# Kernel tuning notes

Measured on AMD Instinct MI355X. Metric: run time of the kernel, lower is better.

The kernel has to match this reference:

```python
import jax, jax.numpy as jnp
import numpy as np

EMBED_DIM = 1024
NUM_HEADS = 16
HEAD_DIM = EMBED_DIM // NUM_HEADS


def setup_inputs() -> dict:
    key = jax.random.key(0)
    ks = jax.random.split(key, 9)
    B, S, D = 2, 2048, EMBED_DIM
    s = 1.0 / np.sqrt(D)
    x = jax.random.normal(ks[0], (B, S, D), dtype=jnp.float32)
    Wq = jax.random.uniform(ks[1], (D, D), jnp.float32, -s, s)
    bq = jax.random.uniform(ks[2], (D,), jnp.float32, -s, s)
    Wk = jax.random.uniform(ks[3], (D, D), jnp.float32, -s, s)
    bk = jax.random.uniform(ks[4], (D,), jnp.float32, -s, s)
    Wv = jax.random.uniform(ks[5], (D, D), jnp.float32, -s, s)
    bv = jax.random.uniform(ks[6], (D,), jnp.float32, -s, s)
    Wo = jax.random.uniform(ks[7], (D, D), jnp.float32, -s, s)
    bo = jax.random.uniform(ks[8], (D,), jnp.float32, -s, s)
    return {"x": x, "Wq": Wq, "bq": bq, "Wk": Wk, "bk": bk,
            "Wv": Wv, "bv": bv, "Wo": Wo, "bo": bo}


def reference(x, Wq, bq, Wk, bk, Wv, bv, Wo, bo):
    B, S, D = x.shape
    H, Hd = NUM_HEADS, HEAD_DIM
    # projections (torch Linear: y = x W^T + b); split heads -> [B, H, S, Hd]
    def split(t):
        return t.reshape(B, S, H, Hd).transpose(0, 2, 1, 3)
    Q = split(x @ Wq.T + bq)
    K = split(x @ Wk.T + bk)
    V = split(x @ Wv.T + bv)
    scores = jnp.einsum('bhqd,bhkd->bhqk', Q, K) / jnp.sqrt(jnp.float32(Hd))
    weights = jax.nn.softmax(scores, axis=-1)
    out = jnp.einsum('bhqk,bhkd->bhqd', weights, V)
    out = out.transpose(0, 2, 1, 3).reshape(B, S, D)
    return out @ Wo.T + bo
```

## Files before the change

kernel.cpp:

```cpp
#include <hip/hip_runtime.h>

typedef float f32x4  __attribute__((ext_vector_type(4)));
typedef float f32x16 __attribute__((ext_vector_type(16)));
typedef short bh8    __attribute__((ext_vector_type(8)));
typedef unsigned int u32;

#define MFMA16(a, b, c) __builtin_amdgcn_mfma_f32_16x16x32_bf16(a, b, c, 0, 0, 0)
#define MFMA32(a, b, c) __builtin_amdgcn_mfma_f32_32x32x16_bf16(a, b, c, 0, 0, 0)

#define BB 2
#define SS 2048
#define DD 1024
#define HH 16
#define HDIM 64
#define TT (BB * SS)

#define QSCALE 0.18033688011f

__device__ __forceinline__ unsigned short f2bf(float f) {
  unsigned u = __float_as_uint(f);
  u += 0x7fffu + ((u >> 16) & 1u);
  return (unsigned short)(u >> 16);
}
__device__ __forceinline__ float bf2f(short h) {
  return __uint_as_float(((u32)(unsigned short)h) << 16);
}
__device__ __forceinline__ u32 cvtpk(float lo, float hi) {
  u32 r;
  asm("v_cvt_pk_bf16_f32 %0, %1, %2" : "=v"(r) : "v"(lo), "v"(hi));
  return r;
}
#define PLSWAP(a, b) \
  asm("v_permlane32_swap_b32 %0, %1" : "+v"(a), "+v"(b))

__device__ __forceinline__ void gload_lds16(const void* gsrc, const void* ldst) {
  __builtin_amdgcn_global_load_lds(
      (const __attribute__((address_space(1))) unsigned int*)(unsigned long long)gsrc,
      (__attribute__((address_space(3))) unsigned int*)(unsigned int)(unsigned long long)ldst,
      16, 0, 0);
}

__global__ void cvt_all(const float* __restrict__ x,
                        const float* __restrict__ w0, const float* __restrict__ w1,
                        const float* __restrict__ w2, const float* __restrict__ w3,
                        unsigned short* __restrict__ xb,
                        unsigned short* __restrict__ wb) {
  const int b = blockIdx.x;
  const float* src;
  unsigned short* dst;
  int i;
  if (b < 2048) {
    src = x; dst = xb;
    i = b * 256 + threadIdx.x;
  } else {
    const int z = (b - 2048) >> 9;
    src = (z == 0) ? w0 : (z == 1) ? w1 : (z == 2) ? w2 : w3;
    dst = wb + (size_t)z * 1048576;
    i = ((b - 2048) & 511) * 256 + threadIdx.x;
  }
  const float4* s = (const float4*)src;
  float4 a = s[i * 2 + 0];
  float4 c = s[i * 2 + 1];
  bh8 v;
  v[0] = (short)f2bf(a.x); v[1] = (short)f2bf(a.y);
  v[2] = (short)f2bf(a.z); v[3] = (short)f2bf(a.w);
  v[4] = (short)f2bf(c.x); v[5] = (short)f2bf(c.y);
  v[6] = (short)f2bf(c.z); v[7] = (short)f2bf(c.w);
  *(bh8*)(dst + (size_t)i * 8) = v;
}

template <int EPI>
__global__ __launch_bounds__(256) void gemm128(
    const unsigned short* __restrict__ A,
    const unsigned short* __restrict__ Bw,
    const float* __restrict__ b0, const float* __restrict__ b1,
    const float* __restrict__ b2,
    unsigned short* __restrict__ Qw, unsigned short* __restrict__ Kw,
    unsigned short* __restrict__ Vtw, float* __restrict__ outf) {
  __shared__ __attribute__((aligned(16))) unsigned short As[2][128 * 32];
  __shared__ __attribute__((aligned(16))) unsigned short Bs[2][128 * 32];

  const int tid = threadIdx.x, lane = tid & 63, wid = tid >> 6;
  const int c = lane & 15, g = lane >> 4;
  const int wr = wid >> 1, wc = wid & 1;
  const int m0 = blockIdx.x * 128, n0 = blockIdx.y * 128;

  const unsigned short* Ab = A + (size_t)(m0 + (lane >> 2)) * DD + (lane & 3) * 8;
  const unsigned short* Bb = Bw + (size_t)(n0 + (lane >> 2)) * DD + (lane & 3) * 8;
  const int rowb0 = wid * 32, rowb1 = wid * 32 + 16;

  f32x4 acc[4][4];
#pragma unroll
  for (int mi = 0; mi < 4; ++mi)
#pragma unroll
    for (int ni = 0; ni < 4; ++ni) acc[mi][ni] = (f32x4){0.f, 0.f, 0.f, 0.f};

  gload_lds16(Ab + (size_t)rowb0 * DD, &As[0][rowb0 * 32]);
  gload_lds16(Ab + (size_t)rowb1 * DD, &As[0][rowb1 * 32]);
  gload_lds16(Bb + (size_t)rowb0 * DD, &Bs[0][rowb0 * 32]);
  gload_lds16(Bb + (size_t)rowb1 * DD, &Bs[0][rowb1 * 32]);
  __syncthreads();

  const int NT = DD / 32;
  for (int t = 0; t < NT; ++t) {
    const int cur = t & 1;
    if (t + 1 < NT) {
      const int k1 = (t + 1) * 32;
      gload_lds16(Ab + (size_t)rowb0 * DD + k1, &As[cur ^ 1][rowb0 * 32]);
      gload_lds16(Ab + (size_t)rowb1 * DD + k1, &As[cur ^ 1][rowb1 * 32]);
      gload_lds16(Bb + (size_t)rowb0 * DD + k1, &Bs[cur ^ 1][rowb0 * 32]);
      gload_lds16(Bb + (size_t)rowb1 * DD + k1, &Bs[cur ^ 1][rowb1 * 32]);
    }

    bh8 a[4], b[4];
#pragma unroll
    for (int mi = 0; mi < 4; ++mi)
      a[mi] = *(const bh8*)&As[cur][(wr * 64 + mi * 16 + c) * 32 + g * 8];
#pragma unroll
    for (int ni = 0; ni < 4; ++ni)
      b[ni] = *(const bh8*)&Bs[cur][(wc * 64 + ni * 16 + c) * 32 + g * 8];
    __builtin_amdgcn_s_setprio(1);
#pragma unroll
    for (int mi = 0; mi < 4; ++mi)
#pragma unroll
      for (int ni = 0; ni < 4; ++ni)
        acc[mi][ni] = MFMA16(a[mi], b[ni], acc[mi][ni]);
    __builtin_amdgcn_s_setprio(0);

    __syncthreads();
  }

  if (EPI == 0) {
#pragma unroll
    for (int ni = 0; ni < 4; ++ni) {
      const int n = n0 + wc * 64 + ni * 16 + c;
      const int z = n >> 10, oo = n & 1023;
      const float bias = (z == 0 ? b0 : (z == 1 ? b1 : b2))[oo];
      const int h = oo >> 6, hd = oo & 63;
#pragma unroll
      for (int mi = 0; mi < 4; ++mi)
#pragma unroll
        for (int j = 0; j < 4; ++j) {
          const int m = m0 + wr * 64 + mi * 16 + g * 4 + j;
          const int bb = m >> 11, s = m & (SS - 1);
          float vv = acc[mi][ni][j] + bias;
          if (z == 0) vv *= QSCALE;
          const unsigned short v = f2bf(vv);
          if (z == 2)
            Vtw[(((size_t)(bb * HH + h) * HDIM + hd) << 11) + s] = v;
          else {
            unsigned short* O = (z == 0) ? Qw : Kw;
            O[(((size_t)(bb * HH + h) * SS + s) << 6) + hd] = v;
          }
        }
    }
  } else {
#pragma unroll
    for (int ni = 0; ni < 4; ++ni) {
      const int n = n0 + wc * 64 + ni * 16 + c;
      const float bias = b0[n];
#pragma unroll
      for (int mi = 0; mi < 4; ++mi)
#pragma unroll
        for (int j = 0; j < 4; ++j) {
          const int m = m0 + wr * 64 + mi * 16 + g * 4 + j;
          outf[(size_t)m * DD + n] = acc[mi][ni][j] + bias;
        }
    }
  }
}

__global__ __launch_bounds__(256, 3) void attn7(
    const unsigned short* __restrict__ Qw, const unsigned short* __restrict__ Kw,
    const unsigned short* __restrict__ Vtw,
    unsigned short* __restrict__ o0, unsigned short* __restrict__ o1,
    float* __restrict__ lbuf) {
  __shared__ __attribute__((aligned(16))) unsigned short KT[2][4096];
  __shared__ __attribute__((aligned(16))) unsigned short VT[2][4096];

  const int f = blockIdx.x;
  const int work = (f & 7) * 128 + (f >> 3);
  const int bx = work & 15;
  const int kvh = (work >> 4) & 1;
  const int bhh = work >> 5;
  const int by = bhh & 15, bz = bhh >> 4;

  const int tid = threadIdx.x;
  const int lane = tid & 63, wid = tid >> 6;
  const int q = lane & 31, hi = lane >> 5;
  const int x7 = lane & 7;
  const int bh = bz * HH + by;
  const unsigned short* Qb = Qw + (size_t)bh * SS * HDIM;
  const unsigned short* Kb = Kw + (size_t)bh * SS * HDIM + (size_t)kvh * 1024 * HDIM;
  const unsigned short* Vb = Vtw + (size_t)bh * HDIM * SS + (size_t)kvh * 1024;
  const int q0 = bx * 128 + wid * 32;

  bh8 qf[4];
#pragma unroll
  for (int ks = 0; ks < 4; ++ks)
    qf[ks] = *(const bh8*)(Qb + (size_t)(q0 + q) * HDIM + ks * 16 + hi * 8);

  f32x16 O0, O1;
#pragma unroll
  for (int r = 0; r < 16; ++r) { O0[r] = 0.f; O1[r] = 0.f; }
  float la[4] = {0.f, 0.f, 0.f, 0.f};

  const int srow = tid >> 2;
  const int c0 = (tid & 3) * 2;
  const int sr7 = srow & 7;
  const int wk0 = srow * 64 + ((c0) ^ sr7) * 8;
  const int wk1 = srow * 64 + ((c0 + 1) ^ sr7) * 8;
  const unsigned short* Ksrc = Kb + (size_t)srow * HDIM + c0 * 8;
  const unsigned short* Vsrc = Vb + (size_t)srow * SS + c0 * 8;

  bh8 kr0 = *(const bh8*)(Ksrc + 0), kr1 = *(const bh8*)(Ksrc + 8);
  bh8 vr0 = *(const bh8*)(Vsrc + 0), vr1 = *(const bh8*)(Vsrc + 8);
  *(bh8*)&KT[0][wk0] = kr0; *(bh8*)&KT[0][wk1] = kr1;
  *(bh8*)&VT[0][wk0] = vr0; *(bh8*)&VT[0][wk1] = vr1;
  kr0 = *(const bh8*)(Ksrc + 64 * HDIM); kr1 = *(const bh8*)(Ksrc + 64 * HDIM + 8);
  vr0 = *(const bh8*)(Vsrc + 64);        vr1 = *(const bh8*)(Vsrc + 64 + 8);

  const int NT = 1024 / 64;
  for (int kt = 0; kt < NT; ++kt) {
    const int cur = kt & 1;
    __syncthreads();
    if (kt + 1 < NT) {
      *(bh8*)&KT[cur ^ 1][wk0] = kr0;
      *(bh8*)&KT[cur ^ 1][wk1] = kr1;
      *(bh8*)&VT[cur ^ 1][wk0] = vr0;
      *(bh8*)&VT[cur ^ 1][wk1] = vr1;
      if (kt + 2 < NT) {
        const size_t ko = (size_t)(kt + 2) * 64 * HDIM, vo = (size_t)(kt + 2) * 64;
        kr0 = *(const bh8*)(Ksrc + ko); kr1 = *(const bh8*)(Ksrc + ko + 8);
        vr0 = *(const bh8*)(Vsrc + vo); vr1 = *(const bh8*)(Vsrc + vo + 8);
      }
    }

#pragma unroll
    for (int kvt = 0; kvt < 2; ++kvt) {
      bh8 kf[4];
#pragma unroll
      for (int ks = 0; ks < 4; ++ks)
        kf[ks] = *(const bh8*)&KT[cur][(kvt * 32 + q) * 64 +
                                       (((ks * 2 + hi) ^ x7) * 8)];
      f32x16 a;
#pragma unroll
      for (int r = 0; r < 16; ++r) a[r] = 0.f;
      __builtin_amdgcn_s_setprio(1);
#pragma unroll
      for (int ks = 0; ks < 4; ++ks) a = MFMA32(kf[ks], qf[ks], a);
      __builtin_amdgcn_s_setprio(0);

      bh8 vf00 = *(const bh8*)&VT[cur][q * 64 + (((kvt * 4 + hi) ^ x7) * 8)];
      bh8 vf01 = *(const bh8*)&VT[cur][(32 + q) * 64 + (((kvt * 4 + hi) ^ x7) * 8)];
      bh8 vf10 = *(const bh8*)&VT[cur][q * 64 + (((kvt * 4 + 2 + hi) ^ x7) * 8)];
      bh8 vf11 = *(const bh8*)&VT[cur][(32 + q) * 64 + (((kvt * 4 + 2 + hi) ^ x7) * 8)];

      u32 w[8];
#pragma unroll
      for (int i = 0; i < 8; ++i) {
        float p0 = __builtin_amdgcn_exp2f(a[2 * i]);
        float p1 = __builtin_amdgcn_exp2f(a[2 * i + 1]);
        la[i & 3] += p0 + p1;
        w[i] = cvtpk(p0, p1);
      }
      PLSWAP(w[0], w[2]); PLSWAP(w[1], w[3]);
      PLSWAP(w[4], w[6]); PLSWAP(w[5], w[7]);

      union { u32 uw[4]; bh8 h; } pa0, pa1;
#pragma unroll
      for (int j = 0; j < 4; ++j) { pa0.uw[j] = w[j]; pa1.uw[j] = w[4 + j]; }
      __builtin_amdgcn_s_setprio(1);
      O0 = MFMA32(vf00, pa0.h, O0);
      O1 = MFMA32(vf01, pa0.h, O1);
      O0 = MFMA32(vf10, pa1.h, O0);
      O1 = MFMA32(vf11, pa1.h, O1);
      __builtin_amdgcn_s_setprio(0);
    }
  }

  float l = (la[0] + la[1]) + (la[2] + la[3]);
  {
    float xa = l, xb = l;
    asm("" : "+v"(xb));
    PLSWAP(xa, xb);
    l = xa + xb;
  }
  if (hi == 0) lbuf[kvh * (BB * HH * SS) + bh * SS + q0 + q] = l;

  unsigned short* orow =
      (kvh ? o1 : o0) + (size_t)(bz * SS + q0 + q) * DD + by * HDIM;
#pragma unroll
  for (int rq = 0; rq < 4; ++rq) {
    const int db0 = 8 * rq + 4 * hi;
    uint2 v0, v1;
    v0.x = cvtpk(O0[4 * rq + 0], O0[4 * rq + 1]);
    v0.y = cvtpk(O0[4 * rq + 2], O0[4 * rq + 3]);
    v1.x = cvtpk(O1[4 * rq + 0], O1[4 * rq + 1]);
    v1.y = cvtpk(O1[4 * rq + 2], O1[4 * rq + 3]);
    *(uint2*)(orow + db0) = v0;
    *(uint2*)(orow + 32 + db0) = v1;
  }
}

__global__ __launch_bounds__(256) void attn_merge(
    const unsigned short* __restrict__ p0, const unsigned short* __restrict__ p1,
    const float* __restrict__ lbuf, unsigned short* outw) {
  const int i = blockIdx.x * blockDim.x + threadIdx.x;
  const int base = i * 8;
  const int row = base >> 10, col = base & 1023;
  const int li = (((row >> 11) << 4) + (col >> 6)) * SS + (row & (SS - 1));
  const float inv = 1.0f / (lbuf[li] + lbuf[BB * HH * SS + li]);
  bh8 a = *(const bh8*)(p0 + base);
  bh8 b = *(const bh8*)(p1 + base);
  bh8 o;
#pragma unroll
  for (int j = 0; j < 8; ++j)
    o[j] = (short)f2bf((bf2f(a[j]) + bf2f(b[j])) * inv);
  *(bh8*)(outw + base) = o;
}

extern "C" void kernel_launch(void* const* d_in, const int* in_sizes, int n_in,
                              void* d_out, int out_size, void* d_ws,
                              size_t ws_size, hipStream_t stream) {
  const float* x  = (const float*)d_in[0];
  const float* Wq = (const float*)d_in[1];
  const float* bq = (const float*)d_in[2];
  const float* Wk = (const float*)d_in[3];
  const float* bk = (const float*)d_in[4];
  const float* Wv = (const float*)d_in[5];
  const float* bv = (const float*)d_in[6];
  const float* Wo = (const float*)d_in[7];
  const float* bo = (const float*)d_in[8];
  float* out = (float*)d_out;

  unsigned short* ws = (unsigned short*)d_ws;
  unsigned short* xb    = ws;
  unsigned short* Wqb   = ws + 4194304;
  unsigned short* Qw    = ws + 8388608;
  unsigned short* Kw    = ws + 12582912;
  unsigned short* Vtw   = ws + 16777216;
  unsigned short* attnw = ws + 20971520;
  float* lbuf = (float*)(ws + 4194304);

  cvt_all<<<dim3(4096), 256, 0, stream>>>(x, Wq, Wk, Wv, Wo, xb, Wqb);

  gemm128<0><<<dim3(TT / 128, 3072 / 128), 256, 0, stream>>>(
      xb, Wqb, bq, bk, bv, Qw, Kw, Vtw, nullptr);

  attn7<<<dim3(1024), 256, 0, stream>>>(Qw, Kw, Vtw, attnw, xb, lbuf);
  attn_merge<<<dim3(TT * DD / 8 / 256), 256, 0, stream>>>(attnw, xb, lbuf, attnw);

  gemm128<1><<<dim3(TT / 128, DD / 128), 256, 0, stream>>>(
      attnw, Wqb + 3 * 1048576, bo, nullptr, nullptr, nullptr, nullptr, nullptr, out);
}
```

Measured before the change: 117.8 us.

## Drop split-KV attention and merge kernel; swizzle GEMM block order across XCDs

The attention kernel no longer splits the key sequence into two halves. Each block now walks all 2048 keys and normalises its output in place, so the separate merge kernel, the partial-output buffers and the l-buffer traffic all go away. The GEMM kernels also remap block indices so consecutive work tiles are spread across the 8 XCDs, aiming for better L2 locality. The cost is that attention launches only 512 blocks instead of 1024, which gives less parallelism and a longer serial loop per block.

Measured after the change: 126.0 us. +6.9%, slower.

```diff
diff --git a/kernel.cpp b/kernel.cpp
--- a/kernel.cpp
+++ b/kernel.cpp
@@ -21,9 +21,6 @@
   unsigned u = __float_as_uint(f);
   u += 0x7fffu + ((u >> 16) & 1u);
   return (unsigned short)(u >> 16);
-}
-__device__ __forceinline__ float bf2f(short h) {
-  return __uint_as_float(((u32)(unsigned short)h) << 16);
 }
 __device__ __forceinline__ u32 cvtpk(float lo, float hi) {
   u32 r;
@@ -80,10 +77,15 @@
   __shared__ __attribute__((aligned(16))) unsigned short As[2][128 * 32];
   __shared__ __attribute__((aligned(16))) unsigned short Bs[2][128 * 32];
 
+  const int total = (EPI == 0) ? 768 : 256;
+  const int flat = blockIdx.y * 32 + blockIdx.x;
+  const int work = (flat & 7) * (total >> 3) + (flat >> 3);
+  const int bx = work & 31, by = work >> 5;
+
   const int tid = threadIdx.x, lane = tid & 63, wid = tid >> 6;
   const int c = lane & 15, g = lane >> 4;
   const int wr = wid >> 1, wc = wid & 1;
-  const int m0 = blockIdx.x * 128, n0 = blockIdx.y * 128;
+  const int m0 = bx * 128, n0 = by * 128;
 
   const unsigned short* Ab = A + (size_t)(m0 + (lane >> 2)) * DD + (lane & 3) * 8;
   const unsigned short* Bb = Bw + (size_t)(n0 + (lane >> 2)) * DD + (lane & 3) * 8;
@@ -170,29 +172,25 @@
   }
 }
 
-__global__ __launch_bounds__(256, 3) void attn7(
+__global__ __launch_bounds__(256, 3) void attn8(
     const unsigned short* __restrict__ Qw, const unsigned short* __restrict__ Kw,
-    const unsigned short* __restrict__ Vtw,
-    unsigned short* __restrict__ o0, unsigned short* __restrict__ o1,
-    float* __restrict__ lbuf) {
+    const unsigned short* __restrict__ Vtw, unsigned short* __restrict__ attnw) {
   __shared__ __attribute__((aligned(16))) unsigned short KT[2][4096];
   __shared__ __attribute__((aligned(16))) unsigned short VT[2][4096];
 
   const int f = blockIdx.x;
-  const int work = (f & 7) * 128 + (f >> 3);
+  const int work = (f & 7) * 64 + (f >> 3);
   const int bx = work & 15;
-  const int kvh = (work >> 4) & 1;
-  const int bhh = work >> 5;
-  const int by = bhh & 15, bz = bhh >> 4;
+  const int bh = work >> 4;
+  const int by = bh & 15, bz = bh >> 4;
 
   const int tid = threadIdx.x;
   const int lane = tid & 63, wid = tid >> 6;
   const int q = lane & 31, hi = lane >> 5;
   const int x7 = lane & 7;
-  const int bh = bz * HH + by;
   const unsigned short* Qb = Qw + (size_t)bh * SS * HDIM;
-  const unsigned short* Kb = Kw + (size_t)bh * SS * HDIM + (size_t)kvh * 1024 * HDIM;
-  const unsigned short* Vb = Vtw + (size_t)bh * HDIM * SS + (size_t)kvh * 1024;
+  const unsigned short* Kb = Kw + (size_t)bh * SS * HDIM;
+  const unsigned short* Vb = Vtw + (size_t)bh * HDIM * SS;
   const int q0 = bx * 128 + wid * 32;
 
   bh8 qf[4];
@@ -220,7 +218,7 @@
   kr0 = *(const bh8*)(Ksrc + 64 * HDIM); kr1 = *(const bh8*)(Ksrc + 64 * HDIM + 8);
   vr0 = *(const bh8*)(Vsrc + 64);        vr1 = *(const bh8*)(Vsrc + 64 + 8);
 
-  const int NT = 1024 / 64;
+  const int NT = SS / 64;
   for (int kt = 0; kt < NT; ++kt) {
     const int cur = kt & 1;
     __syncthreads();
@@ -286,38 +284,20 @@
     PLSWAP(xa, xb);
     l = xa + xb;
   }
-  if (hi == 0) lbuf[kvh * (BB * HH * SS) + bh * SS + q0 + q] = l;
-
+  const float inv = 1.0f / l;
   unsigned short* orow =
-      (kvh ? o1 : o0) + (size_t)(bz * SS + q0 + q) * DD + by * HDIM;
+      attnw + (size_t)(bz * SS + q0 + q) * DD + by * HDIM;
 #pragma unroll
   for (int rq = 0; rq < 4; ++rq) {
     const int db0 = 8 * rq + 4 * hi;
     uint2 v0, v1;
-    v0.x = cvtpk(O0[4 * rq + 0], O0[4 * rq + 1]);
-    v0.y = cvtpk(O0[4 * rq + 2], O0[4 * rq + 3]);
-    v1.x = cvtpk(O1[4 * rq + 0], O1[4 * rq + 1]);
-    v1.y = cvtpk(O1[4 * rq + 2], O1[4 * rq + 3]);
+    v0.x = cvtpk(O0[4 * rq + 0] * inv, O0[4 * rq + 1] * inv);
+    v0.y = cvtpk(O0[4 * rq + 2] * inv, O0[4 * rq + 3] * inv);
+    v1.x = cvtpk(O1[4 * rq + 0] * inv, O1[4 * rq + 1] * inv);
+    v1.y = cvtpk(O1[4 * rq + 2] * inv, O1[4 * rq + 3] * inv);
     *(uint2*)(orow + db0) = v0;
     *(uint2*)(orow + 32 + db0) = v1;
   }
-}
-
-__global__ __launch_bounds__(256) void attn_merge(
-    const unsigned short* __restrict__ p0, const unsigned short* __restrict__ p1,
-    const float* __restrict__ lbuf, unsigned short* outw) {
-  const int i = blockIdx.x * blockDim.x + threadIdx.x;
-  const int base = i * 8;
-  const int row = base >> 10, col = base & 1023;
-  const int li = (((row >> 11) << 4) + (col >> 6)) * SS + (row & (SS - 1));
-  const float inv = 1.0f / (lbuf[li] + lbuf[BB * HH * SS + li]);
-  bh8 a = *(const bh8*)(p0 + base);
-  bh8 b = *(const bh8*)(p1 + base);
-  bh8 o;
-#pragma unroll
-  for (int j = 0; j < 8; ++j)
-    o[j] = (short)f2bf((bf2f(a[j]) + bf2f(b[j])) * inv);
-  *(bh8*)(outw + base) = o;
 }
 
 extern "C" void kernel_launch(void* const* d_in, const int* in_sizes, int n_in,
@@ -341,16 +321,14 @@
   unsigned short* Kw    = ws + 12582912;
   unsigned short* Vtw   = ws + 16777216;
   unsigned short* attnw = ws + 20971520;
-  float* lbuf = (float*)(ws + 4194304);
 
   cvt_all<<<dim3(4096), 256, 0, stream>>>(x, Wq, Wk, Wv, Wo, xb, Wqb);
 
-  gemm128<0><<<dim3(TT / 128, 3072 / 128), 256, 0, stream>>>(
+  gemm128<0><<<dim3(32, 24), 256, 0, stream>>>(
       xb, Wqb, bq, bk, bv, Qw, Kw, Vtw, nullptr);
 
-  attn7<<<dim3(1024), 256, 0, stream>>>(Qw, Kw, Vtw, attnw, xb, lbuf);
-  attn_merge<<<dim3(TT * DD / 8 / 256), 256, 0, stream>>>(attnw, xb, lbuf, attnw);
-
-  gemm128<1><<<dim3(TT / 128, DD / 128), 256, 0, stream>>>(
+  attn8<<<dim3(512), 256, 0, stream>>>(Qw, Kw, Vtw, attnw);
+
+  gemm128<1><<<dim3(32, 8), 256, 0, stream>>>(
       attnw, Wqb + 3 * 1048576, bo, nullptr, nullptr, nullptr, nullptr, nullptr, out);
 }
```
